# Performance work log

Measured on AMD Instinct MI355X. Metric: run time of the kernel, lower is better.

Reference implementation:

```python
import jax, jax.numpy as jnp
import numpy as np

B, T, V = 512, 400, 32000
ENC, HID, EMB = 1024, 1024, 512


def setup_inputs() -> dict:
    key = jax.random.key(0)
    ks = jax.random.split(key, 10)
    vocab_dist = jax.random.uniform(ks[0], (B, V), dtype=jnp.float32)
    vocab_dist = vocab_dist / vocab_dist.sum(-1, keepdims=True)
    attn_dist = jax.random.uniform(ks[1], (B, T), dtype=jnp.float32)
    attn_dist = attn_dist / attn_dist.sum(-1, keepdims=True)
    return {
        "vocab_dist": vocab_dist,
        "attn_dist": attn_dist,
        "context": jax.random.normal(ks[2], (B, ENC), dtype=jnp.float32),
        "state": jax.random.normal(ks[3], (B, HID), dtype=jnp.float32),
        "emb": jax.random.normal(ks[4], (B, EMB), dtype=jnp.float32),
        "src_ids": jax.random.randint(ks[5], (B, T), 0, 32200),
        "vocab_size": V,
        # learned params: w_c: Linear(enc,1), w_s: Linear(hid,1), w_y: Linear(emb,1), bias b
        "w_c": jax.random.normal(ks[6], (ENC,), dtype=jnp.float32) / np.sqrt(ENC),
        "w_s": jax.random.normal(ks[7], (HID,), dtype=jnp.float32) / np.sqrt(HID),
        "w_y": jax.random.normal(ks[8], (EMB,), dtype=jnp.float32) / np.sqrt(EMB),
        "b": jnp.zeros((1,), dtype=jnp.float32),
    }


def reference(vocab_dist, attn_dist, context, state, emb, src_ids, vocab_size, w_c, w_s, w_y, b):
    # p_gen: [B, 1] gating scalar per batch row
    p_gen = jax.nn.sigmoid(
        (context @ w_c + state @ w_s + emb @ w_y)[:, None] + b
    )
    p_vocab = p_gen * vocab_dist                      # [B, V]
    p_copy = (1.0 - p_gen) * attn_dist                # [B, T]
    copy_mask = (src_ids < vocab_size).astype(p_copy.dtype)
    safe_src_ids = jnp.minimum(src_ids, vocab_size - 1)
    rows = jnp.arange(src_ids.shape[0])[:, None]      # [B, 1]
    final_dist = p_vocab.at[rows, safe_src_ids].add(p_copy * copy_mask)
    return final_dist
```

## Files before the change

kernel.cpp:

```cpp
#include <hip/hip_runtime.h>


__global__ __launch_bounds__(256) void pg_gate_kernel(
    const float* __restrict__ context,
    const float* __restrict__ state,
    const float* __restrict__ emb,
    const float* __restrict__ w_c, const float* __restrict__ w_s,
    const float* __restrict__ w_y, const float* __restrict__ bias,
    float* __restrict__ pg,
    int ENC, int HID, int EMB)
{
    const int row = blockIdx.x;
    const int tid = threadIdx.x;
    float acc = 0.f;
    {
        const float4* a4 = (const float4*)(context + (size_t)row * ENC);
        const float4* w4 = (const float4*)w_c;
        for (int i = tid; i < (ENC >> 2); i += 256) {
            float4 a = a4[i], w = w4[i];
            acc += a.x * w.x + a.y * w.y + a.z * w.z + a.w * w.w;
        }
    }
    {
        const float4* a4 = (const float4*)(state + (size_t)row * HID);
        const float4* w4 = (const float4*)w_s;
        for (int i = tid; i < (HID >> 2); i += 256) {
            float4 a = a4[i], w = w4[i];
            acc += a.x * w.x + a.y * w.y + a.z * w.z + a.w * w.w;
        }
    }
    {
        const float4* a4 = (const float4*)(emb + (size_t)row * EMB);
        const float4* w4 = (const float4*)w_y;
        for (int i = tid; i < (EMB >> 2); i += 256) {
            float4 a = a4[i], w = w4[i];
            acc += a.x * w.x + a.y * w.y + a.z * w.z + a.w * w.w;
        }
    }
    #pragma unroll
    for (int off = 32; off > 0; off >>= 1)
        acc += __shfl_down(acc, off, 64);
    __shared__ float red[4];
    if ((tid & 63) == 0) red[tid >> 6] = acc;
    __syncthreads();
    if (tid == 0) {
        float s = red[0] + red[1] + red[2] + red[3] + bias[0];
        pg[row] = 1.f / (1.f + expf(-s));
    }
}

__global__ __launch_bounds__(256) void pg_scale_kernel(
    const float* __restrict__ vocab_dist,
    const float* __restrict__ pg,
    float* __restrict__ out,
    int V)
{
    const int row = blockIdx.y;
    const float p = pg[row];
    const size_t rowV = (size_t)row * V;
    const int nv4 = V >> 2;
    const int i4 = blockIdx.x * 256 + threadIdx.x;
    if (i4 < nv4) {
        float4 v = ((const float4*)(vocab_dist + rowV))[i4];
        v.x *= p; v.y *= p; v.z *= p; v.w *= p;
        ((float4*)(out + rowV))[i4] = v;
    }
    const int tail = V & 3;
    if (blockIdx.x == 0 && threadIdx.x < tail) {
        const int idx = (nv4 << 2) + threadIdx.x;
        out[rowV + idx] = vocab_dist[rowV + idx] * p;
    }
}

__global__ __launch_bounds__(256) void pg_scatter_kernel(
    const float* __restrict__ attn_dist,
    const int*   __restrict__ src_ids,
    const int*   __restrict__ vocab_size_p,
    const float* __restrict__ pg,
    float* __restrict__ out,
    int T, int V)
{
    const int row = blockIdx.y;
    const int t = blockIdx.x * 256 + threadIdx.x;
    if (t >= T) return;
    const int vs = *vocab_size_p;
    const float pc = 1.f - pg[row];
    const int id = src_ids[(size_t)row * T + t];
    if (id < vs)
        atomicAdd(out + (size_t)row * V + id, pc * attn_dist[(size_t)row * T + t]);
}

extern "C" void kernel_launch(void* const* d_in, const int* in_sizes, int n_in,
                              void* d_out, int out_size, void* d_ws, size_t ws_size,
                              hipStream_t stream) {
    const float* vocab_dist = (const float*)d_in[0];
    const float* attn_dist  = (const float*)d_in[1];
    const float* context    = (const float*)d_in[2];
    const float* state      = (const float*)d_in[3];
    const float* emb        = (const float*)d_in[4];
    const int*   src_ids    = (const int*)d_in[5];
    const int*   vocab_sz   = (const int*)d_in[6];
    const float* w_c        = (const float*)d_in[7];
    const float* w_s        = (const float*)d_in[8];
    const float* w_y        = (const float*)d_in[9];
    const float* bias       = (const float*)d_in[10];
    float* out = (float*)d_out;
    float* pg  = (float*)d_ws;

    const int ENC = in_sizes[7];
    const int HID = in_sizes[8];
    const int EMB = in_sizes[9];
    const int B   = in_sizes[2] / ENC;
    const int T   = in_sizes[1] / B;
    const int V   = in_sizes[0] / B;
    const int nv4 = V >> 2;

    pg_gate_kernel<<<B, 256, 0, stream>>>(context, state, emb,
                                          w_c, w_s, w_y, bias, pg,
                                          ENC, HID, EMB);

    dim3 g2((nv4 + 255) / 256, B);
    pg_scale_kernel<<<g2, 256, 0, stream>>>(vocab_dist, pg, out, V);

    dim3 g3((T + 255) / 256, B);
    pg_scatter_kernel<<<g3, 256, 0, stream>>>(attn_dist, src_ids, vocab_sz,
                                              pg, out, T, V);
}
```

Before: 145.8 us.

## Fuse scale and scatter into one kernel using LDS-chunked accumulation

Merges the vocab scaling kernel and the global-atomic scatter kernel into one kernel. Each block owns an 8192-wide vocab chunk of one row, scatters the copy probabilities into shared memory with LDS atomics, then writes out p*vocab + accumulated copy in a single pass. This removes a kernel launch and the global atomic read-modify-write traffic on the output. In exchange, every block re-reads the full src_ids/attn_dist row (4 chunks per row), and the 32KB of LDS per block may limit occupancy.

```diff
diff --git a/kernel.cpp b/kernel.cpp
--- a/kernel.cpp
+++ b/kernel.cpp
@@ -1,5 +1,7 @@
 #include <hip/hip_runtime.h>
 
+
+#define CHUNK 8192
 
 __global__ __launch_bounds__(256) void pg_gate_kernel(
     const float* __restrict__ context,
@@ -49,30 +51,8 @@
     }
 }
 
-__global__ __launch_bounds__(256) void pg_scale_kernel(
+__global__ __launch_bounds__(256) void pg_scale_scatter_kernel(
     const float* __restrict__ vocab_dist,
-    const float* __restrict__ pg,
-    float* __restrict__ out,
-    int V)
-{
-    const int row = blockIdx.y;
-    const float p = pg[row];
-    const size_t rowV = (size_t)row * V;
-    const int nv4 = V >> 2;
-    const int i4 = blockIdx.x * 256 + threadIdx.x;
-    if (i4 < nv4) {
-        float4 v = ((const float4*)(vocab_dist + rowV))[i4];
-        v.x *= p; v.y *= p; v.z *= p; v.w *= p;
-        ((float4*)(out + rowV))[i4] = v;
-    }
-    const int tail = V & 3;
-    if (blockIdx.x == 0 && threadIdx.x < tail) {
-        const int idx = (nv4 << 2) + threadIdx.x;
-        out[rowV + idx] = vocab_dist[rowV + idx] * p;
-    }
-}
-
-__global__ __launch_bounds__(256) void pg_scatter_kernel(
     const float* __restrict__ attn_dist,
     const int*   __restrict__ src_ids,
     const int*   __restrict__ vocab_size_p,
@@ -80,14 +60,49 @@
     float* __restrict__ out,
     int T, int V)
 {
+    __shared__ float lds[CHUNK];
     const int row = blockIdx.y;
-    const int t = blockIdx.x * 256 + threadIdx.x;
-    if (t >= T) return;
-    const int vs = *vocab_size_p;
-    const float pc = 1.f - pg[row];
-    const int id = src_ids[(size_t)row * T + t];
-    if (id < vs)
-        atomicAdd(out + (size_t)row * V + id, pc * attn_dist[(size_t)row * T + t]);
+    const int v0  = blockIdx.x * CHUNK;
+    const int len = min(CHUNK, V - v0);
+    const int tid = threadIdx.x;
+
+    float4* l4 = (float4*)lds;
+    #pragma unroll 4
+    for (int i = tid; i < (CHUNK >> 2); i += 256)
+        l4[i] = make_float4(0.f, 0.f, 0.f, 0.f);
+
+    const float p  = pg[row];
+    const float pc = 1.f - p;
+    const int   vs = *vocab_size_p;
+    __syncthreads();
+
+    const float* at = attn_dist + (size_t)row * T;
+    const int*   si = src_ids  + (size_t)row * T;
+    for (int t = tid; t < T; t += 256) {
+        int id = si[t];
+        if (id < vs) {
+            int off = id - v0;
+            if ((unsigned)off < (unsigned)len)
+                atomicAdd(&lds[off], pc * at[t]);
+        }
+    }
+    __syncthreads();
+
+    const size_t base = (size_t)row * V + v0;
+    const float4* vd4 = (const float4*)(vocab_dist + base);
+    float4*       o4  = (float4*)(out + base);
+    const int n4 = len >> 2;
+    for (int i = tid; i < n4; i += 256) {
+        float4 v = vd4[i];
+        float4 a = l4[i];
+        v.x = v.x * p + a.x;
+        v.y = v.y * p + a.y;
+        v.z = v.z * p + a.z;
+        v.w = v.w * p + a.w;
+        o4[i] = v;
+    }
+    for (int i = (n4 << 2) + tid; i < len; i += 256)
+        out[base + i] = vocab_dist[base + i] * p + lds[i];
 }
 
 extern "C" void kernel_launch(void* const* d_in, const int* in_sizes, int n_in,
@@ -113,16 +128,12 @@
     const int B   = in_sizes[2] / ENC;
     const int T   = in_sizes[1] / B;
     const int V   = in_sizes[0] / B;
-    const int nv4 = V >> 2;
 
     pg_gate_kernel<<<B, 256, 0, stream>>>(context, state, emb,
                                           w_c, w_s, w_y, bias, pg,
                                           ENC, HID, EMB);
 
-    dim3 g2((nv4 + 255) / 256, B);
-    pg_scale_kernel<<<g2, 256, 0, stream>>>(vocab_dist, pg, out, V);
-
-    dim3 g3((T + 255) / 256, B);
-    pg_scatter_kernel<<<g3, 256, 0, stream>>>(attn_dist, src_ids, vocab_sz,
-                                              pg, out, T, V);
+    dim3 g2((V + CHUNK - 1) / CHUNK, B);
+    pg_scale_scatter_kernel<<<g2, 256, 0, stream>>>(
+        vocab_dist, attn_dist, src_ids, vocab_sz, pg, out, T, V);
 }
```

Result: faster. 140.0 us (-4.0%).
